# Kernel optimization log

Measured on AMD Instinct MI355X. Metric: run time of the kernel, lower is better.

The kernel has to match this reference:

```python
import jax, jax.numpy as jnp
import numpy as np

VOCAB = 50257
E = 1024
CTX = 1024
C = 50
NEG = 10


def setup_inputs() -> dict:
    key = jax.random.key(0)
    ks = jax.random.split(key, 10)
    return {
        "x": jax.random.randint(ks[0], (1,), 0, VOCAB),
        "context": jax.random.randint(ks[1], (C,), 0, VOCAB),
        "neg_samples": jax.random.randint(ks[2], (C, NEG), 0, VOCAB),
        "emb": jax.random.normal(ks[3], (VOCAB, E), jnp.float32) * 0.02,
        "M_w": jax.random.normal(ks[4], (CTX, E), jnp.float32) * 0.02,
        "M_b": jnp.zeros((CTX,), jnp.float32),
        "U_w": jax.random.normal(ks[5], (CTX, 2 * CTX), jnp.float32) * 0.02,
        "U_b": jnp.zeros((CTX,), jnp.float32),
        "W_w": jax.random.normal(ks[6], (CTX, 2 * CTX), jnp.float32) * 0.02,
        "W_b": jnp.zeros((CTX,), jnp.float32),
        "prior_mus": jax.random.normal(ks[7], (VOCAB, CTX), jnp.float32) * 0.02,
        # keep sigmas away from 0 so log(sigma^2) is well-behaved
        "prior_sigmas": jax.random.uniform(ks[8], (VOCAB, CTX), jnp.float32, 0.5, 1.5),
    }


def reference(x, context, neg_samples, emb, M_w, M_b, U_w, U_b, W_w, W_b,
              prior_mus, prior_sigmas):
    c_len = context.shape[0]
    # Rw: Embedding(x) [1,E] repeated to [C,E], then M (Linear E->CTX)
    Rw = emb[x] @ M_w.T + M_b                       # [1, CTX]
    Rw = jnp.broadcast_to(Rw, (c_len, Rw.shape[-1]))  # [C, CTX]
    Rc = emb[context] @ M_w.T + M_b                 # [C, CTX]
    h = jax.nn.relu(jnp.concatenate([Rw, Rc], axis=1)).sum(0)  # [2*CTX]
    mu = U_w @ h + U_b                              # [CTX]
    # NOTE: posterior covariance is diag(sigma), NOT diag(sigma^2)
    sigma = jax.nn.softplus(W_w @ h + W_b)          # [CTX]

    k = mu.shape[0]
    log_det_p = jnp.sum(jnp.log(sigma))

    def kl_post_to(m, s2):
        # KL( N(mu, diag(sigma)) || N(m, diag(s2)) ), batched over leading dims
        return 0.5 * (jnp.sum((sigma + (m - mu) ** 2) / s2 + jnp.log(s2), axis=-1)
                      - k - log_det_p)

    kl_pos = kl_post_to(prior_mus[context], prior_sigmas[context] ** 2)        # [C]
    kl_neg = kl_post_to(prior_mus[neg_samples], prior_sigmas[neg_samples] ** 2)  # [C, NEG]
    likelihood = jnp.maximum(0.0, kl_neg - kl_pos[:, None] + 1.0).sum()
    kl_prior = kl_post_to(prior_mus[x], prior_sigmas[x] ** 2)                  # [1]
    return likelihood - kl_prior
```

## Files before the change

kernel.cpp:

```cpp
#include <hip/hip_runtime.h>
#include <math.h>

#define EDIM 1024
#define CTXDIM 1024
#define H2 2048


#define ALD(p) __hip_atomic_load((p), __ATOMIC_RELAXED, __HIP_MEMORY_SCOPE_AGENT)

__global__ __launch_bounds__(1024) void k_h(
    const float* __restrict__ emb, const float* __restrict__ Mw,
    const float* __restrict__ Mb, const int* __restrict__ x,
    const int* __restrict__ ctx, int C, int CN, float* __restrict__ ws)
{
    __shared__ int   idxs[64];
    __shared__ float pacc[16];
    __shared__ float pxs[4];
    const int tid  = threadIdx.x;
    const int w    = tid >> 6;
    const int lane = tid & 63;
    const int c    = w & 3;
    const int g    = w >> 2;
    const int j    = blockIdx.x * 4 + c;

    if (blockIdx.x == 0 && tid < 8 + 2 + C + CN)
        ws[4096 + tid] = 0.f;
    if (tid <= C) idxs[tid] = (tid == 0) ? x[0] : ctx[tid - 1];

    const float4* mrow = (const float4*)(Mw + (size_t)j * EDIM);
    const float4 mw0 = mrow[lane];
    const float4 mw1 = mrow[lane + 64];
    const float4 mw2 = mrow[lane + 128];
    const float4 mw3 = mrow[lane + 192];
    const float bj = Mb[j];
    __syncthreads();

    float acc = 0.f, px = 0.f;
#pragma unroll 2
    for (int r = g; r <= C; r += 4) {
        const int idx = idxs[r];
        const float4* e4 = (const float4*)(emb + (size_t)idx * EDIM);
        const float4 a  = e4[lane];
        const float4 bb = e4[lane + 64];
        const float4 d  = e4[lane + 128];
        const float4 e  = e4[lane + 192];
        float s = a.x*mw0.x + a.y*mw0.y + a.z*mw0.z + a.w*mw0.w;
        s += bb.x*mw1.x + bb.y*mw1.y + bb.z*mw1.z + bb.w*mw1.w;
        s += d.x*mw2.x + d.y*mw2.y + d.z*mw2.z + d.w*mw2.w;
        s += e.x*mw3.x + e.y*mw3.y + e.z*mw3.z + e.w*mw3.w;
#pragma unroll
        for (int m = 32; m >= 1; m >>= 1) s += __shfl_xor(s, m);
        const float v = fmaxf(s + bj, 0.f);
        if (r == 0) px = (float)C * v;
        else        acc += v;
    }
    if (lane == 0) {
        pacc[w] = acc;
        if (g == 0) pxs[c] = px;
    }
    __syncthreads();
    if (tid < 4) {
        const int jj = blockIdx.x * 4 + tid;
        ws[jj]          = pxs[tid];
        ws[CTXDIM + jj] = pacc[tid] + pacc[tid + 4] + pacc[tid + 8] + pacc[tid + 12];
    }
}

__global__ __launch_bounds__(1024) void k_tail(
    const float* __restrict__ Uw, const float* __restrict__ Ub,
    const float* __restrict__ Ww, const float* __restrict__ Wb,
    const float* __restrict__ pmu, const float* __restrict__ psig,
    const int* __restrict__ x, const int* __restrict__ ctx,
    const int* __restrict__ negs, int C, int CN, int NEG, int KDIM,
    int nblk, float* __restrict__ ws, float* __restrict__ out)
{
    __shared__ float4 hbuf4[512];
    __shared__ float  msig[16];
    __shared__ int    winflag;
    const int tid  = threadIdx.x;
    const int w    = tid >> 6;
    const int lane = tid & 63;
    const int b    = blockIdx.x;
    float* Sbuf    = ws + 4100;
    unsigned* cnt  = (unsigned*)(ws + 4096);

    const int nkl = 1 + C + CN;
    float4 gm0, gm1, gs0, gs1;
    if (tid < nkl) {
        const int idx = (tid == 0) ? x[0]
                       : (tid <= C ? ctx[tid - 1] : negs[tid - 1 - C]);
        const float4* m4 = (const float4*)(pmu  + (size_t)idx * CTXDIM + 8 * b);
        const float4* s4 = (const float4*)(psig + (size_t)idx * CTXDIM + 8 * b);
        gm0 = m4[0]; gm1 = m4[1];
        gs0 = s4[0]; gs1 = s4[1];
    }

    if (tid < 512) hbuf4[tid] = ((const float4*)ws)[tid];
    __syncthreads();

    {
        const int colw = w & 7;
        const int i = 8 * b + colw;
        const float4* W4 = (const float4*)(((w < 8) ? Uw : Ww) + (size_t)i * H2);
        float s = 0.f;
#pragma unroll
        for (int k = 0; k < 8; ++k) {
            const float4 wv = W4[lane + 64 * k];
            const float4 hv = hbuf4[lane + 64 * k];
            s += wv.x*hv.x + wv.y*hv.y + wv.z*hv.z + wv.w*hv.w;
        }
#pragma unroll
        for (int m = 32; m >= 1; m >>= 1) s += __shfl_xor(s, m);
        if (lane == 0) {
            if (w < 8) {
                msig[colw] = s + Ub[i];
            } else {
                const float v = s + Wb[i];
                msig[8 + colw] = fmaxf(v, 0.f) + log1pf(expf(-fabsf(v)));
            }
        }
    }
    __syncthreads();

    if (tid < nkl) {
        const float mu0 = msig[0], mu1 = msig[1], mu2 = msig[2], mu3 = msig[3];
        const float mu4 = msig[4], mu5 = msig[5], mu6 = msig[6], mu7 = msig[7];
        const float sg0 = msig[8], sg1 = msig[9], sg2 = msig[10], sg3 = msig[11];
        const float sg4 = msig[12], sg5 = msig[13], sg6 = msig[14], sg7 = msig[15];
        float acc = 0.f;
        { const float s2 = gs0.x*gs0.x; const float d = gm0.x - mu0; acc += (sg0 + d*d)/s2 + logf(s2); }
        { const float s2 = gs0.y*gs0.y; const float d = gm0.y - mu1; acc += (sg1 + d*d)/s2 + logf(s2); }
        { const float s2 = gs0.z*gs0.z; const float d = gm0.z - mu2; acc += (sg2 + d*d)/s2 + logf(s2); }
        { const float s2 = gs0.w*gs0.w; const float d = gm0.w - mu3; acc += (sg3 + d*d)/s2 + logf(s2); }
        { const float s2 = gs1.x*gs1.x; const float d = gm1.x - mu4; acc += (sg4 + d*d)/s2 + logf(s2); }
        { const float s2 = gs1.y*gs1.y; const float d = gm1.y - mu5; acc += (sg5 + d*d)/s2 + logf(s2); }
        { const float s2 = gs1.z*gs1.z; const float d = gm1.z - mu6; acc += (sg6 + d*d)/s2 + logf(s2); }
        { const float s2 = gs1.w*gs1.w; const float d = gm1.w - mu7; acc += (sg7 + d*d)/s2 + logf(s2); }
        atomicAdd(&Sbuf[1 + tid], acc);
    } else if (tid == nkl) {
        float ld = 0.f;
#pragma unroll
        for (int jj = 0; jj < 8; ++jj) ld += logf(msig[8 + jj]);
        atomicAdd(&Sbuf[0], ld);
    }

    __syncthreads();
    if (tid == 0) {
        const unsigned old = __hip_atomic_fetch_add(cnt, 1u,
                               __ATOMIC_RELEASE, __HIP_MEMORY_SCOPE_AGENT);
        winflag = (old == (unsigned)(nblk - 1));
    }
    __syncthreads();
    if (winflag && w == 0) {
        __builtin_amdgcn_fence(__ATOMIC_ACQUIRE, "agent");
        float lik = 0.f;
        for (int i = lane; i < CN; i += 64) {
            const float sn = ALD(&Sbuf[2 + C + i]);
            const float sp = ALD(&Sbuf[2 + i / NEG]);
            lik += fmaxf(0.f, 0.5f * (sn - sp) + 1.0f);
        }
#pragma unroll
        for (int m = 32; m >= 1; m >>= 1) lik += __shfl_xor(lik, m);
        if (lane == 0) {
            const float ld = ALD(&Sbuf[0]);
            const float sx = ALD(&Sbuf[1]);
            out[0] = lik - 0.5f * (sx - (float)KDIM - ld);
        }
    }
}

extern "C" void kernel_launch(void* const* d_in, const int* in_sizes, int n_in,
                              void* d_out, int out_size, void* d_ws, size_t ws_size,
                              hipStream_t stream) {
    const int*   x    = (const int*)d_in[0];
    const int*   ctx  = (const int*)d_in[1];
    const int*   negs = (const int*)d_in[2];
    const float* emb  = (const float*)d_in[3];
    const float* Mw   = (const float*)d_in[4];
    const float* Mb   = (const float*)d_in[5];
    const float* Uw   = (const float*)d_in[6];
    const float* Ub   = (const float*)d_in[7];
    const float* Ww   = (const float*)d_in[8];
    const float* Wb   = (const float*)d_in[9];
    const float* pmu  = (const float*)d_in[10];
    const float* psig = (const float*)d_in[11];
    float* ws  = (float*)d_ws;
    float* out = (float*)d_out;

    const int C    = in_sizes[1];
    const int CN   = in_sizes[2];
    const int NEG  = CN / C;
    const int KDIM = in_sizes[5];

    k_h<<<CTXDIM / 4, 1024, 0, stream>>>(emb, Mw, Mb, x, ctx, C, CN, ws);
    k_tail<<<CTXDIM / 8, 1024, 0, stream>>>(Uw, Ub, Ww, Wb, pmu, psig,
                                            x, ctx, negs, C, CN, NEG, KDIM,
                                            CTXDIM / 8, ws, out);
}
```

Before: 30.19 us.

## Spread KL atomics across 16 partial-sum copies and double tail grid

The tail kernel now launches 256 blocks of 512 threads, each handling 4 output columns instead of 8. Per-sample KL partial sums are spread over 16 replicated buffers selected by block index, which reduces atomic contention on the same addresses. The last block sums the copies into shared memory before computing the final loss. In exchange the first kernel has to zero a larger workspace region, the final block does more reduction work, and each block reads the same number of prior rows but uses half as many columns from each.

```diff
diff --git a/kernel.cpp b/kernel.cpp
--- a/kernel.cpp
+++ b/kernel.cpp
@@ -4,6 +4,9 @@
 #define EDIM 1024
 #define CTXDIM 1024
 #define H2 2048
+#define NCOPY 16
+#define CSTRIDE 576
+#define SBASE 4112
 
 
 #define ALD(p) __hip_atomic_load((p), __ATOMIC_RELAXED, __HIP_MEMORY_SCOPE_AGENT)
@@ -11,7 +14,7 @@
 __global__ __launch_bounds__(1024) void k_h(
     const float* __restrict__ emb, const float* __restrict__ Mw,
     const float* __restrict__ Mb, const int* __restrict__ x,
-    const int* __restrict__ ctx, int C, int CN, float* __restrict__ ws)
+    const int* __restrict__ ctx, int C, float* __restrict__ ws)
 {
     __shared__ int   idxs[64];
     __shared__ float pacc[16];
@@ -23,8 +26,10 @@
     const int g    = w >> 2;
     const int j    = blockIdx.x * 4 + c;
 
-    if (blockIdx.x == 0 && tid < 8 + 2 + C + CN)
-        ws[4096 + tid] = 0.f;
+    if (blockIdx.x == 0) {
+        for (int i = tid; i < NCOPY * CSTRIDE + 16; i += 1024)
+            ws[4096 + i] = 0.f;
+    }
     if (tid <= C) idxs[tid] = (tid == 0) ? x[0] : ctx[tid - 1];
 
     const float4* mrow = (const float4*)(Mw + (size_t)j * EDIM);
@@ -66,7 +71,7 @@
     }
 }
 
-__global__ __launch_bounds__(1024) void k_tail(
+__global__ __launch_bounds__(512) void k_tail(
     const float* __restrict__ Uw, const float* __restrict__ Ub,
     const float* __restrict__ Ww, const float* __restrict__ Wb,
     const float* __restrict__ pmu, const float* __restrict__ psig,
@@ -75,33 +80,38 @@
     int nblk, float* __restrict__ ws, float* __restrict__ out)
 {
     __shared__ float4 hbuf4[512];
-    __shared__ float  msig[16];
+    __shared__ float  msig[8];
+    __shared__ float  SL[553];
     __shared__ int    winflag;
     const int tid  = threadIdx.x;
     const int w    = tid >> 6;
     const int lane = tid & 63;
     const int b    = blockIdx.x;
-    float* Sbuf    = ws + 4100;
     unsigned* cnt  = (unsigned*)(ws + 4096);
 
     const int nkl = 1 + C + CN;
-    float4 gm0, gm1, gs0, gs1;
-    if (tid < nkl) {
-        const int idx = (tid == 0) ? x[0]
-                       : (tid <= C ? ctx[tid - 1] : negs[tid - 1 - C]);
-        const float4* m4 = (const float4*)(pmu  + (size_t)idx * CTXDIM + 8 * b);
-        const float4* s4 = (const float4*)(psig + (size_t)idx * CTXDIM + 8 * b);
-        gm0 = m4[0]; gm1 = m4[1];
-        gs0 = s4[0]; gs1 = s4[1];
-    }
-
-    if (tid < 512) hbuf4[tid] = ((const float4*)ws)[tid];
+    const int t0 = tid, t1 = tid + 512;
+    const bool has0 = (t0 < nkl);
+    const bool has1 = (t1 < nkl);
+    float4 gm0, gs0, gm1, gs1;
+    if (has0) {
+        const int idx = (t0 == 0) ? x[0]
+                       : (t0 <= C ? ctx[t0 - 1] : negs[t0 - 1 - C]);
+        gm0 = *(const float4*)(pmu  + (size_t)idx * CTXDIM + 4 * b);
+        gs0 = *(const float4*)(psig + (size_t)idx * CTXDIM + 4 * b);
+    }
+    if (has1) {
+        const int idx = (t1 <= C) ? ctx[t1 - 1] : negs[t1 - 1 - C];
+        gm1 = *(const float4*)(pmu  + (size_t)idx * CTXDIM + 4 * b);
+        gs1 = *(const float4*)(psig + (size_t)idx * CTXDIM + 4 * b);
+    }
+
+    hbuf4[tid] = ((const float4*)ws)[tid];
     __syncthreads();
 
     {
-        const int colw = w & 7;
-        const int i = 8 * b + colw;
-        const float4* W4 = (const float4*)(((w < 8) ? Uw : Ww) + (size_t)i * H2);
+        const int col = 4 * b + (w & 3);
+        const float4* W4 = (const float4*)(((w < 4) ? Uw : Ww) + (size_t)col * H2);
         float s = 0.f;
 #pragma unroll
         for (int k = 0; k < 8; ++k) {
@@ -112,36 +122,37 @@
 #pragma unroll
         for (int m = 32; m >= 1; m >>= 1) s += __shfl_xor(s, m);
         if (lane == 0) {
-            if (w < 8) {
-                msig[colw] = s + Ub[i];
+            if (w < 4) {
+                msig[w & 3] = s + Ub[col];
             } else {
-                const float v = s + Wb[i];
-                msig[8 + colw] = fmaxf(v, 0.f) + log1pf(expf(-fabsf(v)));
+                const float v = s + Wb[col];
+                msig[4 + (w & 3)] = fmaxf(v, 0.f) + log1pf(expf(-fabsf(v)));
             }
         }
     }
     __syncthreads();
 
-    if (tid < nkl) {
-        const float mu0 = msig[0], mu1 = msig[1], mu2 = msig[2], mu3 = msig[3];
-        const float mu4 = msig[4], mu5 = msig[5], mu6 = msig[6], mu7 = msig[7];
-        const float sg0 = msig[8], sg1 = msig[9], sg2 = msig[10], sg3 = msig[11];
-        const float sg4 = msig[12], sg5 = msig[13], sg6 = msig[14], sg7 = msig[15];
+    float* copy = ws + SBASE + (size_t)(b & (NCOPY - 1)) * CSTRIDE;
+    const float mu0 = msig[0], mu1 = msig[1], mu2 = msig[2], mu3 = msig[3];
+    const float sg0 = msig[4], sg1 = msig[5], sg2 = msig[6], sg3 = msig[7];
+    if (has0) {
         float acc = 0.f;
         { const float s2 = gs0.x*gs0.x; const float d = gm0.x - mu0; acc += (sg0 + d*d)/s2 + logf(s2); }
         { const float s2 = gs0.y*gs0.y; const float d = gm0.y - mu1; acc += (sg1 + d*d)/s2 + logf(s2); }
         { const float s2 = gs0.z*gs0.z; const float d = gm0.z - mu2; acc += (sg2 + d*d)/s2 + logf(s2); }
         { const float s2 = gs0.w*gs0.w; const float d = gm0.w - mu3; acc += (sg3 + d*d)/s2 + logf(s2); }
-        { const float s2 = gs1.x*gs1.x; const float d = gm1.x - mu4; acc += (sg4 + d*d)/s2 + logf(s2); }
-        { const float s2 = gs1.y*gs1.y; const float d = gm1.y - mu5; acc += (sg5 + d*d)/s2 + logf(s2); }
-        { const float s2 = gs1.z*gs1.z; const float d = gm1.z - mu6; acc += (sg6 + d*d)/s2 + logf(s2); }
-        { const float s2 = gs1.w*gs1.w; const float d = gm1.w - mu7; acc += (sg7 + d*d)/s2 + logf(s2); }
-        atomicAdd(&Sbuf[1 + tid], acc);
-    } else if (tid == nkl) {
-        float ld = 0.f;
-#pragma unroll
-        for (int jj = 0; jj < 8; ++jj) ld += logf(msig[8 + jj]);
-        atomicAdd(&Sbuf[0], ld);
+        atomicAdd(&copy[1 + t0], acc);
+    }
+    if (has1) {
+        float acc = 0.f;
+        { const float s2 = gs1.x*gs1.x; const float d = gm1.x - mu0; acc += (sg0 + d*d)/s2 + logf(s2); }
+        { const float s2 = gs1.y*gs1.y; const float d = gm1.y - mu1; acc += (sg1 + d*d)/s2 + logf(s2); }
+        { const float s2 = gs1.z*gs1.z; const float d = gm1.z - mu2; acc += (sg2 + d*d)/s2 + logf(s2); }
+        { const float s2 = gs1.w*gs1.w; const float d = gm1.w - mu3; acc += (sg3 + d*d)/s2 + logf(s2); }
+        atomicAdd(&copy[1 + t1], acc);
+    } else if (t1 == nkl) {
+        const float ld = logf(sg0) + logf(sg1) + logf(sg2) + logf(sg3);
+        atomicAdd(&copy[0], ld);
     }
 
     __syncthreads();
@@ -151,21 +162,28 @@
         winflag = (old == (unsigned)(nblk - 1));
     }
     __syncthreads();
-    if (winflag && w == 0) {
-        __builtin_amdgcn_fence(__ATOMIC_ACQUIRE, "agent");
+    if (!winflag) return;
+
+    __builtin_amdgcn_fence(__ATOMIC_ACQUIRE, "agent");
+    for (int t = tid; t < 2 + C + CN; t += 512) {
+        float sfull = 0.f;
+#pragma unroll
+        for (int cc = 0; cc < NCOPY; ++cc)
+            sfull += ALD(&ws[SBASE + cc * CSTRIDE + t]);
+        SL[t] = sfull;
+    }
+    __syncthreads();
+    if (w == 0) {
         float lik = 0.f;
         for (int i = lane; i < CN; i += 64) {
-            const float sn = ALD(&Sbuf[2 + C + i]);
-            const float sp = ALD(&Sbuf[2 + i / NEG]);
+            const float sn = SL[2 + C + i];
+            const float sp = SL[2 + i / NEG];
             lik += fmaxf(0.f, 0.5f * (sn - sp) + 1.0f);
         }
 #pragma unroll
         for (int m = 32; m >= 1; m >>= 1) lik += __shfl_xor(lik, m);
-        if (lane == 0) {
-            const float ld = ALD(&Sbuf[0]);
-            const float sx = ALD(&Sbuf[1]);
-            out[0] = lik - 0.5f * (sx - (float)KDIM - ld);
-        }
+        if (lane == 0)
+            out[0] = lik - 0.5f * (SL[1] - (float)KDIM - SL[0]);
     }
 }
 
@@ -192,8 +210,8 @@
     const int NEG  = CN / C;
     const int KDIM = in_sizes[5];
 
-    k_h<<<CTXDIM / 4, 1024, 0, stream>>>(emb, Mw, Mb, x, ctx, C, CN, ws);
-    k_tail<<<CTXDIM / 8, 1024, 0, stream>>>(Uw, Ub, Ww, Wb, pmu, psig,
-                                            x, ctx, negs, C, CN, NEG, KDIM,
-                                            CTXDIM / 8, ws, out);
+    k_h<<<CTXDIM / 4, 1024, 0, stream>>>(emb, Mw, Mb, x, ctx, C, ws);
+    k_tail<<<CTXDIM / 4, 512, 0, stream>>>(Uw, Ub, Ww, Wb, pmu, psig,
+                                           x, ctx, negs, C, CN, NEG, KDIM,
+                                           CTXDIM / 4, ws, out);
 }
```

Result: slower. 32.18 us (+6.6%).
